# Performance work log

Measured on AMD Instinct MI355X. Metric: run time of the kernel, lower is better.

The kernel has to match this reference:

```python
import jax, jax.numpy as jnp
import numpy as np

IN_F, OUT_F, N_TOK = 4096, 4096, 8192

def setup_inputs() -> dict:
    key = jax.random.key(0)
    k1, k2, k3, k4, k5 = jax.random.split(key, 5)
    bound = 1.0 / np.sqrt(IN_F)  # kaiming_uniform-ish scale for mean, uniform for bias
    x = jax.random.normal(k1, (N_TOK, IN_F), dtype=jnp.float32)
    mean = jax.random.uniform(k2, (OUT_F, IN_F), minval=-bound, maxval=bound, dtype=jnp.float32)
    sigma = jax.random.uniform(k3, (OUT_F, IN_F), minval=0.05, maxval=0.2, dtype=jnp.float32)
    bias = jax.random.uniform(k4, (OUT_F,), minval=-bound, maxval=bound, dtype=jnp.float32)
    # uniform[-1, 1] noise matrix (torch init.uniform_(w, a=-1, b=1))
    noise = jax.random.uniform(k5, (OUT_F, IN_F), minval=-1.0, maxval=1.0, dtype=jnp.float32)
    sigma_mult = 2  # discrete bucket multiplier in {1, 2, 4}
    return {"x": x, "mean": mean, "sigma": sigma, "bias": bias, "noise": noise, "sigma_mult": sigma_mult}

def reference(x, mean, sigma, bias, noise, sigma_mult):
    # w = mean * (1 + noise * |sigma| * sigma_mult), then F.linear(x, w, bias) = x @ w.T + bias
    w = mean * (1.0 + noise * jnp.abs(sigma) * sigma_mult)  # [out, in]
    return jnp.einsum('ti,oi->to', x, w) + bias
```

## Files before the change

kernel.cpp:

```cpp
#include <hip/hip_runtime.h>
#include <hip/hip_bf16.h>

#define M_TOK 8192
#define N_OUT 4096
#define K_IN  4096
#define NT    64

typedef __attribute__((ext_vector_type(8))) short bf16x8;
typedef __attribute__((ext_vector_type(4))) float f32x4;
typedef unsigned short u16;

__device__ static inline u16 f2bf(float f) {
    union { float f; unsigned int u; } v; v.f = f;
    unsigned int u = v.u;
    u += 0x7FFFu + ((u >> 16) & 1u);
    return (u16)(u >> 16);
}

__device__ static inline void load_lds16(const void* g, void* l) {
    __builtin_amdgcn_global_load_lds(
        (const __attribute__((address_space(1))) unsigned int*)g,
        (__attribute__((address_space(3))) unsigned int*)l,
        16, 0, 0);
}

__global__ void prep_kernel(const float* __restrict__ x,
                            const float* __restrict__ mean,
                            const float* __restrict__ sigma,
                            const float* __restrict__ noise,
                            const int* __restrict__ smult,
                            u16* __restrict__ xb, u16* __restrict__ wb) {
    if (blockIdx.x < 2048) {
        const int n4 = (M_TOK * K_IN) / 4;
        int i = blockIdx.x * blockDim.x + threadIdx.x;
        const int stride = 2048 * 256;
        for (int e = i; e < n4; e += stride) {
            float4 v = reinterpret_cast<const float4*>(x)[e];
            ushort4 o;
            o.x = f2bf(v.x); o.y = f2bf(v.y); o.z = f2bf(v.z); o.w = f2bf(v.w);
            reinterpret_cast<ushort4*>(xb)[e] = o;
        }
    } else {
        const float sm = (float)(*smult);
        const int n4 = (N_OUT * K_IN) / 4;
        int i = (blockIdx.x - 2048) * blockDim.x + threadIdx.x;
        const int stride = 1024 * 256;
        for (int e = i; e < n4; e += stride) {
            float4 m = reinterpret_cast<const float4*>(mean)[e];
            float4 s = reinterpret_cast<const float4*>(sigma)[e];
            float4 z = reinterpret_cast<const float4*>(noise)[e];
            ushort4 o;
            o.x = f2bf(m.x * (1.0f + z.x * fabsf(s.x) * sm));
            o.y = f2bf(m.y * (1.0f + z.y * fabsf(s.y) * sm));
            o.z = f2bf(m.z * (1.0f + z.z * fabsf(s.z) * sm));
            o.w = f2bf(m.w * (1.0f + z.w * fabsf(s.w) * sm));
            reinterpret_cast<ushort4*>(wb)[e] = o;
        }
    }
}


#define BAR()   __builtin_amdgcn_s_barrier()
#define LGKM0() asm volatile("s_waitcnt lgkmcnt(0)" ::: "memory")
#define VMC4()  asm volatile("s_waitcnt vmcnt(4)" ::: "memory")
#define VMC0()  asm volatile("s_waitcnt vmcnt(0)" ::: "memory")

#define DS_A4(AR, MG, AB) \
  _Pragma("unroll") for (int m_ = 0; m_ < 4; ++m_) { \
    AR[m_][0] = *reinterpret_cast<const bf16x8*>((AB) + ((MG)+m_)*1024 + aoff0); \
    AR[m_][1] = *reinterpret_cast<const bf16x8*>((AB) + ((MG)+m_)*1024 + aoff1); }

#define DS_B2(BR, NG, BB) \
  _Pragma("unroll") for (int n_ = 0; n_ < 2; ++n_) { \
    BR[n_][0] = *reinterpret_cast<const bf16x8*>((BB) + ((NG)+n_)*1024 + aoff0); \
    BR[n_][1] = *reinterpret_cast<const bf16x8*>((BB) + ((NG)+n_)*1024 + aoff1); }

#define QUAD(MG, NG, AR, BR) \
  __builtin_amdgcn_s_setprio(1); \
  _Pragma("unroll") for (int m_ = 0; m_ < 4; ++m_) \
  _Pragma("unroll") for (int n_ = 0; n_ < 2; ++n_) { \
    acc[(MG)+m_][(NG)+n_] = __builtin_amdgcn_mfma_f32_16x16x32_bf16( \
        AR[m_][0], BR[n_][0], acc[(MG)+m_][(NG)+n_], 0, 0, 0); \
    acc[(MG)+m_][(NG)+n_] = __builtin_amdgcn_mfma_f32_16x16x32_bf16( \
        AR[m_][1], BR[n_][1], acc[(MG)+m_][(NG)+n_], 0, 0, 0); } \
  __builtin_amdgcn_s_setprio(0);

#define STAGE_A(T, H, BUF) { \
  const u16* g_ = Abase + (size_t)((H)*128 + srow) * K_IN + (T)*64 + sxcol; \
  load_lds16(g_, smem + (BUF)*32768 + (H)*8192 + tid*8); \
  load_lds16(g_ + (size_t)64*K_IN, smem + (BUF)*32768 + (H)*8192 + 4096 + tid*8); }

#define STAGE_B(T, H, BUF) { \
  const u16* g_ = Bbase + (size_t)((H)*128 + srow) * K_IN + (T)*64 + sxcol; \
  load_lds16(g_, smem + (BUF)*32768 + 16384 + (H)*8192 + tid*8); \
  load_lds16(g_ + (size_t)64*K_IN, smem + (BUF)*32768 + 16384 + (H)*8192 + 4096 + tid*8); }

__global__ __launch_bounds__(512, 2)
void gemm_bias_kernel(const u16* __restrict__ A, const u16* __restrict__ B,
                      const float* __restrict__ bias, float* __restrict__ C) {
    __shared__ u16 smem[65536];

    const int tid   = threadIdx.x;
    const int lane  = tid & 63;
    const int wid   = tid >> 6;
    const int wm    = wid >> 2;
    const int wn    = wid & 3;
    const int la_lo = lane & 15;
    const int la_hi = lane >> 4;

    const int bid = blockIdx.x;
    const int xcd = bid & 7;
    const int c   = bid >> 3;
    const int r   = c >> 5;
    const int s   = c & 31;
    const int bm  = xcd * 4 + (s & 3);
    const int bn  = r * 8 + (s >> 2);
    const int brow = bm * 256;
    const int bcol = bn * 256;

    const u16* Abase = A + (size_t)brow * K_IN;
    const u16* Bbase = B + (size_t)bcol * K_IN;

    const int srow  = tid >> 3;
    const int sxcol = ((tid & 7) ^ (srow & 7)) * 8;

    const int xorr  = la_lo & 7;
    const int aoff0 = la_lo * 64 + ((la_hi    ) ^ xorr) * 8;
    const int aoff1 = la_lo * 64 + ((la_hi + 4) ^ xorr) * 8;

    const u16* A0 = smem +         wm * 8192;
    const u16* A1 = smem + 32768 + wm * 8192;
    const u16* B0 = smem +         16384 + (wn >> 1) * 8192 + (wn & 1) * 4096;
    const u16* B1 = smem + 32768 + 16384 + (wn >> 1) * 8192 + (wn & 1) * 4096;

    f32x4 acc[8][4];
    #pragma unroll
    for (int m = 0; m < 8; ++m)
        #pragma unroll
        for (int n = 0; n < 4; ++n)
            acc[m][n] = (f32x4){0.f, 0.f, 0.f, 0.f};

    bf16x8 aR[4][2], bA[2][2], bB[2][2];

    STAGE_B(0, 0, 0); STAGE_B(0, 1, 0);
    STAGE_A(0, 0, 0); STAGE_A(0, 1, 0);
    STAGE_B(1, 0, 1); STAGE_B(1, 1, 1);
    VMC4();
    BAR();

    for (int i = 0; i < 31; ++i) {
        const int t1 = 2 * i + 1, t2 = 2 * i + 2, t3 = 2 * i + 3;
        DS_A4(aR, 0, A0); DS_B2(bA, 0, B0); STAGE_A(t1, 0, 1);
        BAR(); LGKM0(); QUAD(0, 0, aR, bA); BAR();
        DS_B2(bB, 2, B0); STAGE_A(t1, 1, 1);
        BAR(); LGKM0(); QUAD(0, 2, aR, bB); BAR();
        DS_A4(aR, 4, A0); STAGE_B(t2, 0, 0);
        BAR(); LGKM0(); QUAD(4, 2, aR, bB); BAR();
        STAGE_B(t2, 1, 0);
        BAR(); QUAD(4, 0, aR, bA); VMC4(); BAR();
        DS_A4(aR, 0, A1); DS_B2(bA, 0, B1); STAGE_A(t2, 0, 0);
        BAR(); LGKM0(); QUAD(0, 0, aR, bA); BAR();
        DS_B2(bB, 2, B1); STAGE_A(t2, 1, 0);
        BAR(); LGKM0(); QUAD(0, 2, aR, bB); BAR();
        DS_A4(aR, 4, A1); STAGE_B(t3, 0, 1);
        BAR(); LGKM0(); QUAD(4, 2, aR, bB); BAR();
        STAGE_B(t3, 1, 1);
        BAR(); QUAD(4, 0, aR, bA); VMC4(); BAR();
    }

    DS_A4(aR, 0, A0); DS_B2(bA, 0, B0); STAGE_A(63, 0, 1);
    BAR(); LGKM0(); QUAD(0, 0, aR, bA); BAR();
    DS_B2(bB, 2, B0); STAGE_A(63, 1, 1);
    BAR(); LGKM0(); QUAD(0, 2, aR, bB); BAR();
    DS_A4(aR, 4, A0);
    BAR(); LGKM0(); QUAD(4, 2, aR, bB); BAR();
    BAR(); QUAD(4, 0, aR, bA); VMC0(); BAR();
    DS_A4(aR, 0, A1); DS_B2(bA, 0, B1);
    BAR(); LGKM0(); QUAD(0, 0, aR, bA); BAR();
    DS_B2(bB, 2, B1);
    BAR(); LGKM0(); QUAD(0, 2, aR, bB); BAR();
    DS_A4(aR, 4, A1);
    BAR(); LGKM0(); QUAD(4, 2, aR, bB); BAR();
    QUAD(4, 0, aR, bA);

    const int crow0 = brow + wm * 128;
    const int ccol0 = bcol + wn * 64;
    #pragma unroll
    for (int n = 0; n < 4; ++n) {
        const int col = ccol0 + n * 16 + la_lo;
        const float bv = bias[col];
        #pragma unroll
        for (int m = 0; m < 8; ++m) {
            #pragma unroll
            for (int rr = 0; rr < 4; ++rr) {
                const int row = crow0 + m * 16 + la_hi * 4 + rr;
                C[(size_t)row * N_OUT + col] = acc[m][n][rr] + bv;
            }
        }
    }
}

extern "C" void kernel_launch(void* const* d_in, const int* in_sizes, int n_in,
                              void* d_out, int out_size, void* d_ws, size_t ws_size,
                              hipStream_t stream) {
    const float* x     = (const float*)d_in[0];
    const float* mean  = (const float*)d_in[1];
    const float* sigma = (const float*)d_in[2];
    const float* bias  = (const float*)d_in[3];
    const float* noise = (const float*)d_in[4];
    const int*   smult = (const int*)d_in[5];
    float* out = (float*)d_out;

    const size_t x_elems = (size_t)M_TOK * K_IN;
    const size_t w_elems = (size_t)N_OUT * K_IN;
    const size_t need = (x_elems + w_elems) * sizeof(u16);
    if (ws_size < need) return;

    u16* xb = (u16*)d_ws;
    u16* wb = xb + x_elems;

    prep_kernel<<<3072, 256, 0, stream>>>(x, mean, sigma, noise, smult, xb, wb);
    gemm_bias_kernel<<<512, 512, 0, stream>>>(xb, wb, bias, out);
}
```

Baseline: 313.7 us.

## Switch GEMM to 32x32x16 MFMA with register-prefetched LDS fragments

```diff
diff --git a/kernel.cpp b/kernel.cpp
--- a/kernel.cpp
+++ b/kernel.cpp
@@ -4,10 +4,9 @@
 #define M_TOK 8192
 #define N_OUT 4096
 #define K_IN  4096
-#define NT    64
 
 typedef __attribute__((ext_vector_type(8))) short bf16x8;
-typedef __attribute__((ext_vector_type(4))) float f32x4;
+typedef __attribute__((ext_vector_type(16))) float f32x16;
 typedef unsigned short u16;
 
 __device__ static inline u16 f2bf(float f) {
@@ -60,29 +59,29 @@
 }
 
 
-#define BAR()   __builtin_amdgcn_s_barrier()
-#define LGKM0() asm volatile("s_waitcnt lgkmcnt(0)" ::: "memory")
+#define BAR()    __builtin_amdgcn_s_barrier()
+#define SCHED0() __builtin_amdgcn_sched_barrier(0)
 #define VMC4()  asm volatile("s_waitcnt vmcnt(4)" ::: "memory")
+#define VMC2()  asm volatile("s_waitcnt vmcnt(2)" ::: "memory")
 #define VMC0()  asm volatile("s_waitcnt vmcnt(0)" ::: "memory")
 
-#define DS_A4(AR, MG, AB) \
-  _Pragma("unroll") for (int m_ = 0; m_ < 4; ++m_) { \
-    AR[m_][0] = *reinterpret_cast<const bf16x8*>((AB) + ((MG)+m_)*1024 + aoff0); \
-    AR[m_][1] = *reinterpret_cast<const bf16x8*>((AB) + ((MG)+m_)*1024 + aoff1); }
-
-#define DS_B2(BR, NG, BB) \
-  _Pragma("unroll") for (int n_ = 0; n_ < 2; ++n_) { \
-    BR[n_][0] = *reinterpret_cast<const bf16x8*>((BB) + ((NG)+n_)*1024 + aoff0); \
-    BR[n_][1] = *reinterpret_cast<const bf16x8*>((BB) + ((NG)+n_)*1024 + aoff1); }
-
-#define QUAD(MG, NG, AR, BR) \
+#define LD_A(DST, PAIR, AB) \
+  _Pragma("unroll") for (int mt_ = 0; mt_ < 2; ++mt_) \
+  _Pragma("unroll") for (int kc_ = 0; kc_ < 4; ++kc_) \
+    DST[mt_][kc_] = *reinterpret_cast<const bf16x8*>( \
+      (AB) + (((PAIR)*2 + mt_)*32 + r31)*64 + koffE[kc_]);
+
+#define LD_B(DST, NTT, BB) \
+  _Pragma("unroll") for (int kc_ = 0; kc_ < 4; ++kc_) \
+    DST[kc_] = *reinterpret_cast<const bf16x8*>( \
+      (BB) + ((NTT)*32 + r31)*64 + koffE[kc_]);
+
+#define OCT(MP, NTT, AR, BR) \
   __builtin_amdgcn_s_setprio(1); \
-  _Pragma("unroll") for (int m_ = 0; m_ < 4; ++m_) \
-  _Pragma("unroll") for (int n_ = 0; n_ < 2; ++n_) { \
-    acc[(MG)+m_][(NG)+n_] = __builtin_amdgcn_mfma_f32_16x16x32_bf16( \
-        AR[m_][0], BR[n_][0], acc[(MG)+m_][(NG)+n_], 0, 0, 0); \
-    acc[(MG)+m_][(NG)+n_] = __builtin_amdgcn_mfma_f32_16x16x32_bf16( \
-        AR[m_][1], BR[n_][1], acc[(MG)+m_][(NG)+n_], 0, 0, 0); } \
+  _Pragma("unroll") for (int kc_ = 0; kc_ < 4; ++kc_) \
+  _Pragma("unroll") for (int mt_ = 0; mt_ < 2; ++mt_) \
+    acc[(MP)*2 + mt_][NTT] = __builtin_amdgcn_mfma_f32_32x32x16_bf16( \
+      AR[mt_][kc_], BR[kc_], acc[(MP)*2 + mt_][NTT], 0, 0, 0); \
   __builtin_amdgcn_s_setprio(0);
 
 #define STAGE_A(T, H, BUF) { \
@@ -100,13 +99,14 @@
                       const float* __restrict__ bias, float* __restrict__ C) {
     __shared__ u16 smem[65536];
 
-    const int tid   = threadIdx.x;
-    const int lane  = tid & 63;
-    const int wid   = tid >> 6;
-    const int wm    = wid >> 2;
-    const int wn    = wid & 3;
-    const int la_lo = lane & 15;
-    const int la_hi = lane >> 4;
+    const int tid  = threadIdx.x;
+    const int lane = tid & 63;
+    const int wid  = tid >> 6;
+    const int wm   = wid >> 2;
+    const int wn   = wid & 3;
+    const int r31  = lane & 31;
+    const int hi5  = lane >> 5;
+    const int xr   = lane & 7;
 
     const int bid = blockIdx.x;
     const int xcd = bid & 7;
@@ -124,77 +124,82 @@
     const int srow  = tid >> 3;
     const int sxcol = ((tid & 7) ^ (srow & 7)) * 8;
 
-    const int xorr  = la_lo & 7;
-    const int aoff0 = la_lo * 64 + ((la_hi    ) ^ xorr) * 8;
-    const int aoff1 = la_lo * 64 + ((la_hi + 4) ^ xorr) * 8;
+    int koffE[4];
+    #pragma unroll
+    for (int kc = 0; kc < 4; ++kc)
+        koffE[kc] = ((kc * 2 + hi5) ^ xr) * 8;
 
     const u16* A0 = smem +         wm * 8192;
     const u16* A1 = smem + 32768 + wm * 8192;
     const u16* B0 = smem +         16384 + (wn >> 1) * 8192 + (wn & 1) * 4096;
     const u16* B1 = smem + 32768 + 16384 + (wn >> 1) * 8192 + (wn & 1) * 4096;
 
-    f32x4 acc[8][4];
+    f32x16 acc[4][2];
     #pragma unroll
-    for (int m = 0; m < 8; ++m)
+    for (int m = 0; m < 4; ++m)
         #pragma unroll
-        for (int n = 0; n < 4; ++n)
-            acc[m][n] = (f32x4){0.f, 0.f, 0.f, 0.f};
-
-    bf16x8 aR[4][2], bA[2][2], bB[2][2];
+        for (int n = 0; n < 2; ++n)
+            #pragma unroll
+            for (int e = 0; e < 16; ++e)
+                acc[m][n][e] = 0.f;
+
+    bf16x8 aRe[2][4], aRo[2][4], bA0[4], bA1[4], bB[4];
 
     STAGE_B(0, 0, 0); STAGE_B(0, 1, 0);
     STAGE_A(0, 0, 0); STAGE_A(0, 1, 0);
     STAGE_B(1, 0, 1); STAGE_B(1, 1, 1);
-    VMC4();
-    BAR();
+    VMC4(); BAR();
+    LD_A(aRe, 0, A0); LD_B(bA0, 0, B0);
 
     for (int i = 0; i < 31; ++i) {
         const int t1 = 2 * i + 1, t2 = 2 * i + 2, t3 = 2 * i + 3;
-        DS_A4(aR, 0, A0); DS_B2(bA, 0, B0); STAGE_A(t1, 0, 1);
-        BAR(); LGKM0(); QUAD(0, 0, aR, bA); BAR();
-        DS_B2(bB, 2, B0); STAGE_A(t1, 1, 1);
-        BAR(); LGKM0(); QUAD(0, 2, aR, bB); BAR();
-        DS_A4(aR, 4, A0); STAGE_B(t2, 0, 0);
-        BAR(); LGKM0(); QUAD(4, 2, aR, bB); BAR();
-        STAGE_B(t2, 1, 0);
-        BAR(); QUAD(4, 0, aR, bA); VMC4(); BAR();
-        DS_A4(aR, 0, A1); DS_B2(bA, 0, B1); STAGE_A(t2, 0, 0);
-        BAR(); LGKM0(); QUAD(0, 0, aR, bA); BAR();
-        DS_B2(bB, 2, B1); STAGE_A(t2, 1, 0);
-        BAR(); LGKM0(); QUAD(0, 2, aR, bB); BAR();
-        DS_A4(aR, 4, A1); STAGE_B(t3, 0, 1);
-        BAR(); LGKM0(); QUAD(4, 2, aR, bB); BAR();
-        STAGE_B(t3, 1, 1);
-        BAR(); QUAD(4, 0, aR, bA); VMC4(); BAR();
+        LD_B(bB, 1, B0); STAGE_A(t1, 0, 1);
+        SCHED0(); OCT(0, 0, aRe, bA0); BAR();
+        LD_A(aRo, 1, A0); STAGE_A(t1, 1, 1);
+        SCHED0(); OCT(0, 1, aRe, bB); BAR();
+        STAGE_B(t2, 0, 0);
+        SCHED0(); OCT(1, 1, aRo, bB); VMC2(); BAR();
+        LD_A(aRe, 0, A1); LD_B(bA1, 0, B1); STAGE_B(t2, 1, 0);
+        SCHED0(); OCT(1, 0, aRo, bA0); BAR();
+        LD_B(bB, 1, B1); STAGE_A(t2, 0, 0);
+        SCHED0(); OCT(0, 0, aRe, bA1); BAR();
+        LD_A(aRo, 1, A1); STAGE_A(t2, 1, 0);
+        SCHED0(); OCT(0, 1, aRe, bB); BAR();
+        STAGE_B(t3, 0, 1);
+        SCHED0(); OCT(1, 1, aRo, bB); VMC2(); BAR();
+        LD_A(aRe, 0, A0); LD_B(bA0, 0, B0); STAGE_B(t3, 1, 1);
+        SCHED0(); OCT(1, 0, aRo, bA1); BAR();
     }
 
-    DS_A4(aR, 0, A0); DS_B2(bA, 0, B0); STAGE_A(63, 0, 1);
-    BAR(); LGKM0(); QUAD(0, 0, aR, bA); BAR();
-    DS_B2(bB, 2, B0); STAGE_A(63, 1, 1);
-    BAR(); LGKM0(); QUAD(0, 2, aR, bB); BAR();
-    DS_A4(aR, 4, A0);
-    BAR(); LGKM0(); QUAD(4, 2, aR, bB); BAR();
-    BAR(); QUAD(4, 0, aR, bA); VMC0(); BAR();
-    DS_A4(aR, 0, A1); DS_B2(bA, 0, B1);
-    BAR(); LGKM0(); QUAD(0, 0, aR, bA); BAR();
-    DS_B2(bB, 2, B1);
-    BAR(); LGKM0(); QUAD(0, 2, aR, bB); BAR();
-    DS_A4(aR, 4, A1);
-    BAR(); LGKM0(); QUAD(4, 2, aR, bB); BAR();
-    QUAD(4, 0, aR, bA);
+    LD_B(bB, 1, B0); STAGE_A(63, 0, 1);
+    SCHED0(); OCT(0, 0, aRe, bA0); BAR();
+    LD_A(aRo, 1, A0); STAGE_A(63, 1, 1);
+    SCHED0(); OCT(0, 1, aRe, bB); BAR();
+    SCHED0(); OCT(1, 1, aRo, bB); VMC0(); BAR();
+    LD_A(aRe, 0, A1); LD_B(bA1, 0, B1);
+    SCHED0(); OCT(1, 0, aRo, bA0); BAR();
+    LD_B(bB, 1, B1);
+    SCHED0(); OCT(0, 0, aRe, bA1); BAR();
+    LD_A(aRo, 1, A1);
+    SCHED0(); OCT(0, 1, aRe, bB); BAR();
+    SCHED0(); OCT(1, 1, aRo, bB); BAR();
+    OCT(1, 0, aRo, bA1);
 
     const int crow0 = brow + wm * 128;
     const int ccol0 = bcol + wn * 64;
     #pragma unroll
-    for (int n = 0; n < 4; ++n) {
-        const int col = ccol0 + n * 16 + la_lo;
+    for (int nt = 0; nt < 2; ++nt) {
+        const int col = ccol0 + nt * 32 + r31;
         const float bv = bias[col];
         #pragma unroll
-        for (int m = 0; m < 8; ++m) {
+        for (int mt = 0; mt < 4; ++mt) {
             #pragma unroll
-            for (int rr = 0; rr < 4; ++rr) {
-                const int row = crow0 + m * 16 + la_hi * 4 + rr;
-                C[(size_t)row * N_OUT + col] = acc[m][n][rr] + bv;
+            for (int g = 0; g < 4; ++g) {
+                #pragma unroll
+                for (int rr = 0; rr < 4; ++rr) {
+                    const int row = crow0 + mt * 32 + g * 8 + 4 * hi5 + rr;
+                    C[(size_t)row * N_OUT + col] = acc[mt][nt][g * 4 + rr] + bv;
+                }
             }
         }
     }
```

Measured after the change: 329.3 us. 1.05x slower.

## Software-pipeline LDS fragment loads one phase ahead of MFMA quads

Applied to the files above, without the earlier changes.

```diff
diff --git a/kernel.cpp b/kernel.cpp
--- a/kernel.cpp
+++ b/kernel.cpp
@@ -4,7 +4,6 @@
 #define M_TOK 8192
 #define N_OUT 4096
 #define K_IN  4096
-#define NT    64
 
 typedef __attribute__((ext_vector_type(8))) short bf16x8;
 typedef __attribute__((ext_vector_type(4))) float f32x4;
@@ -60,7 +59,8 @@
 }
 
 
-#define BAR()   __builtin_amdgcn_s_barrier()
+#define BAR()    __builtin_amdgcn_s_barrier()
+#define SCHED0() __builtin_amdgcn_sched_barrier(0)
 #define LGKM0() asm volatile("s_waitcnt lgkmcnt(0)" ::: "memory")
 #define VMC4()  asm volatile("s_waitcnt vmcnt(4)" ::: "memory")
 #define VMC0()  asm volatile("s_waitcnt vmcnt(0)" ::: "memory")
@@ -140,48 +140,50 @@
         for (int n = 0; n < 4; ++n)
             acc[m][n] = (f32x4){0.f, 0.f, 0.f, 0.f};
 
-    bf16x8 aR[4][2], bA[2][2], bB[2][2];
+    bf16x8 aE0[4][2], aO0[4][2], aE1[4][2], aO1[4][2];
+    bf16x8 bA0[2][2], bB0[2][2], bA1[2][2], bB1[2][2];
 
     STAGE_B(0, 0, 0); STAGE_B(0, 1, 0);
     STAGE_A(0, 0, 0); STAGE_A(0, 1, 0);
     STAGE_B(1, 0, 1); STAGE_B(1, 1, 1);
-    VMC4();
+    VMC4(); BAR();
+    SCHED0();
+    DS_A4(aE0, 0, A0); DS_B2(bA0, 0, B0); STAGE_A(1, 0, 1);
     BAR();
 
     for (int i = 0; i < 31; ++i) {
         const int t1 = 2 * i + 1, t2 = 2 * i + 2, t3 = 2 * i + 3;
-        DS_A4(aR, 0, A0); DS_B2(bA, 0, B0); STAGE_A(t1, 0, 1);
-        BAR(); LGKM0(); QUAD(0, 0, aR, bA); BAR();
-        DS_B2(bB, 2, B0); STAGE_A(t1, 1, 1);
-        BAR(); LGKM0(); QUAD(0, 2, aR, bB); BAR();
-        DS_A4(aR, 4, A0); STAGE_B(t2, 0, 0);
-        BAR(); LGKM0(); QUAD(4, 2, aR, bB); BAR();
-        STAGE_B(t2, 1, 0);
-        BAR(); QUAD(4, 0, aR, bA); VMC4(); BAR();
-        DS_A4(aR, 0, A1); DS_B2(bA, 0, B1); STAGE_A(t2, 0, 0);
-        BAR(); LGKM0(); QUAD(0, 0, aR, bA); BAR();
-        DS_B2(bB, 2, B1); STAGE_A(t2, 1, 0);
-        BAR(); LGKM0(); QUAD(0, 2, aR, bB); BAR();
-        DS_A4(aR, 4, A1); STAGE_B(t3, 0, 1);
-        BAR(); LGKM0(); QUAD(4, 2, aR, bB); BAR();
-        STAGE_B(t3, 1, 1);
-        BAR(); QUAD(4, 0, aR, bA); VMC4(); BAR();
+        SCHED0(); DS_B2(bB0, 2, B0); STAGE_A(t1, 1, 1);
+        SCHED0(); QUAD(0, 0, aE0, bA0); LGKM0(); BAR();
+        SCHED0(); DS_A4(aO0, 4, A0); STAGE_B(t2, 0, 0);
+        SCHED0(); QUAD(0, 2, aE0, bB0); BAR();
+        SCHED0(); STAGE_B(t2, 1, 0);
+        SCHED0(); QUAD(4, 2, aO0, bB0); VMC4(); BAR();
+        SCHED0(); DS_A4(aE1, 0, A1); DS_B2(bA1, 0, B1); STAGE_A(t2, 0, 0);
+        SCHED0(); QUAD(4, 0, aO0, bA0); BAR();
+        SCHED0(); DS_B2(bB1, 2, B1); STAGE_A(t2, 1, 0);
+        SCHED0(); QUAD(0, 0, aE1, bA1); LGKM0(); BAR();
+        SCHED0(); DS_A4(aO1, 4, A1); STAGE_B(t3, 0, 1);
+        SCHED0(); QUAD(0, 2, aE1, bB1); BAR();
+        SCHED0(); STAGE_B(t3, 1, 1);
+        SCHED0(); QUAD(4, 2, aO1, bB1); VMC4(); BAR();
+        SCHED0(); DS_A4(aE0, 0, A0); DS_B2(bA0, 0, B0); STAGE_A(t3, 0, 1);
+        SCHED0(); QUAD(4, 0, aO1, bA1); BAR();
     }
 
-    DS_A4(aR, 0, A0); DS_B2(bA, 0, B0); STAGE_A(63, 0, 1);
-    BAR(); LGKM0(); QUAD(0, 0, aR, bA); BAR();
-    DS_B2(bB, 2, B0); STAGE_A(63, 1, 1);
-    BAR(); LGKM0(); QUAD(0, 2, aR, bB); BAR();
-    DS_A4(aR, 4, A0);
-    BAR(); LGKM0(); QUAD(4, 2, aR, bB); BAR();
-    BAR(); QUAD(4, 0, aR, bA); VMC0(); BAR();
-    DS_A4(aR, 0, A1); DS_B2(bA, 0, B1);
-    BAR(); LGKM0(); QUAD(0, 0, aR, bA); BAR();
-    DS_B2(bB, 2, B1);
-    BAR(); LGKM0(); QUAD(0, 2, aR, bB); BAR();
-    DS_A4(aR, 4, A1);
-    BAR(); LGKM0(); QUAD(4, 2, aR, bB); BAR();
-    QUAD(4, 0, aR, bA);
+    SCHED0(); DS_B2(bB0, 2, B0); STAGE_A(63, 1, 1);
+    SCHED0(); QUAD(0, 0, aE0, bA0); LGKM0(); BAR();
+    SCHED0(); DS_A4(aO0, 4, A0);
+    SCHED0(); QUAD(0, 2, aE0, bB0); BAR();
+    SCHED0(); QUAD(4, 2, aO0, bB0); VMC0(); BAR();
+    SCHED0(); DS_A4(aE1, 0, A1); DS_B2(bA1, 0, B1);
+    SCHED0(); QUAD(4, 0, aO0, bA0); BAR();
+    SCHED0(); DS_B2(bB1, 2, B1);
+    SCHED0(); QUAD(0, 0, aE1, bA1); BAR();
+    SCHED0(); DS_A4(aO1, 4, A1);
+    SCHED0(); QUAD(0, 2, aE1, bB1); BAR();
+    SCHED0(); QUAD(4, 2, aO1, bB1); BAR();
+    QUAD(4, 0, aO1, bA1);
 
     const int crow0 = brow + wm * 128;
     const int ccol0 = bcol + wn * 64;
```

Result: slower. 426.5 us (+35.9%).
